# Performance work log

Hardware: AMD Instinct MI355X
Metric: run time of the kernel (lower is better)

## Reference

```python
import jax, jax.numpy as jnp
import numpy as np

N_NODES = 20000
IN_CH = 128
OUT_CH = 128
HEADS = 1
OB_DIM = 4
N_STEP = 32           # = HEADS*OUT_CH*8 // 32
D_PE = 16             # 32 - HEADS*16
N_EDGES = 256000


def setup_inputs() -> dict:
    key = jax.random.key(0)
    ks = jax.random.split(key, 9)
    x = jax.random.normal(ks[0], (N_NODES, IN_CH), jnp.float32)
    p_t = jax.random.normal(ks[1], (N_STEP, D_PE), jnp.float32)
    edge_index = jax.random.randint(ks[2], (2, N_EDGES), 0, N_NODES, jnp.int32)
    edge_weights = jax.random.uniform(ks[3], (N_EDGES,), jnp.float32)
    # Linear params (PyTorch default init: U(-1/sqrt(fan_in), 1/sqrt(fan_in)))
    s = 1.0 / np.sqrt(IN_CH)
    lin_value_w = jax.random.uniform(ks[4], (IN_CH, HEADS * OUT_CH), jnp.float32, -s, s)
    lin_value_b = jax.random.uniform(ks[5], (HEADS * OUT_CH,), jnp.float32, -s, s)
    inc_w = jax.random.uniform(ks[6], (IN_CH, HEADS * OUT_CH * 8), jnp.float32, -s, s)
    inc_b = jax.random.uniform(ks[7], (HEADS * OUT_CH * 8,), jnp.float32, -s, s)
    g = np.sqrt(6.0 / (N_NODES + HEADS * 16))  # glorot
    map_weights = jax.random.uniform(ks[8], (N_NODES, HEADS * 16), jnp.float32, -g, g)
    return {"x": x, "p_t": p_t, "edge_index": edge_index, "edge_weights": edge_weights,
            "lin_value_w": lin_value_w, "lin_value_b": lin_value_b,
            "inc_w": inc_w, "inc_b": inc_b, "map_weights": map_weights}


def _segment_softmax(gamma, index, num_segments):
    # PyG-style softmax over edges grouped by destination index, per column
    m = jax.ops.segment_max(gamma, index, num_segments=num_segments)     # [N, D]
    num = jnp.exp(gamma - m[index])
    den = jax.ops.segment_sum(num, index, num_segments=num_segments)    # [N, D]
    return num / den[index]


def reference(x, p_t, edge_index, edge_weights, lin_value_w, lin_value_b,
              inc_w, inc_b, map_weights):
    src = edge_index[0]   # x_j side
    dst = edge_index[1]   # x_i side (flow source_to_target)
    n_step = p_t.shape[0]
    E = src.shape[0]

    x_i = x[dst]                                             # [E, in]
    # h_W = increase_dim(x_i).view(E, n_step, 32)
    h_W = (x_i @ inc_w + inc_b).reshape(E, n_step, 32)       # [E, T, 32]
    w_v = map_weights[dst]                                   # [E, 16]
    # beta = mean(h_W * cat([w_v, p_t], -1), -1) computed without materializing aa
    beta = (jnp.einsum('etk,ek->et', h_W[:, :, :16], w_v)
            + jnp.einsum('etk,tk->et', h_W[:, :, 16:], p_t)) / 32.0   # [E, T]

    gamma = beta * edge_weights[:, None]                     # [E, T]
    gamma = jnp.repeat(gamma, OB_DIM, axis=-1)               # [E, T*ob_dim] = [E, H*out]
    all_edge_weights = jnp.mean(gamma, axis=1)               # [E]

    K = int(E * 0.5)
    _, top_idx = jax.lax.top_k(all_edge_weights, K)          # top-K edges
    gamma = gamma[top_idx]                                   # [K, H*out]
    x_i = x_i[top_idx]                                       # [K, in]
    # NOTE: the module re-points aggregation index to edge_index[0] (source)
    index = src[top_idx]                                     # [K]

    gamma = _segment_softmax(gamma, index, N_NODES)          # [K, H*out]

    v = jax.nn.relu(x_i @ lin_value_w + lin_value_b)         # [K, H*out]
    msg = (v.reshape(K, HEADS, OUT_CH)
           * gamma.reshape(K, HEADS, OUT_CH))                # [K, H, out]

    out = jax.ops.segment_sum(msg.reshape(K, HEADS * OUT_CH), index,
                              num_segments=N_NODES)          # scatter-add
    return out                                               # [N, H*out]
```

## Files before the change

kernel.cpp:

```cpp
#include <hip/hip_runtime.h>

#define NN 20000
#define IC 128
#define OC 128
#define NSTEP 32
#define NE 256000
#define KSEL 128000
#define NB 79
#define CANDCAP 131072
#define NQCOL 704

struct SelState {
  unsigned long long prefix;
  unsigned r;
  unsigned selc;
  unsigned tiec;
  unsigned done[8];
};

typedef __attribute__((ext_vector_type(16))) float f16v;

__global__ void k_init(const float* __restrict__ p_t, const float* __restrict__ lin_w,
                       const float* __restrict__ lin_b,
                       const float* __restrict__ inc_w, const float* __restrict__ inc_b,
                       float* __restrict__ Wq,
                       double* __restrict__ Ud, double* __restrict__ ubd,
                       unsigned* __restrict__ cnt, unsigned* __restrict__ hist,
                       SelState* st) {
  int i = blockIdx.x * blockDim.x + threadIdx.x;
  if (i < 33 * NQCOL) {
    int k4 = i / NQCOL, col = i - k4 * NQCOL;
    float4 o;
    float* ov = (float*)&o;
    for (int jj = 0; jj < 4; ++jj) {
      int k = 4 * k4 + jj;
      float v = 0.f;
      if (col < 512) {
        int t = col >> 4, c = col & 15;
        if (k < 128) v = inc_w[k * 1024 + t * 32 + c];
        else if (k == 128) v = inc_b[t * 32 + c];
      } else if (col < 544) {
        int t = col - 512;
        if (k < 128) {
          float a = 0.f;
          for (int q = 0; q < 16; ++q) a += inc_w[k * 1024 + t * 32 + 16 + q] * p_t[t * 16 + q];
          v = a;
        } else if (k == 128) {
          float a = 0.f;
          for (int q = 0; q < 16; ++q) a += inc_b[t * 32 + 16 + q] * p_t[t * 16 + q];
          v = a;
        }
      } else if (col < 672) {
        int c = col - 544;
        if (k < 128) v = lin_w[k * OC + c];
        else if (k == 128) v = lin_b[c];
      }
      ov[jj] = v;
    }
    ((float4*)Wq)[i] = o;
    return;
  }
  i -= 33 * NQCOL;
  if (i < 17 * IC) {
    int c = i >> 7, k = i & 127;
    double a = 0.0;
    if (c < 16) {
      for (int t = 0; t < NSTEP; ++t) a += (double)inc_w[k * 1024 + t * 32 + c];
    } else {
      for (int t = 0; t < NSTEP; ++t)
        for (int q = 0; q < 16; ++q)
          a += (double)inc_w[k * 1024 + t * 32 + 16 + q] * (double)p_t[t * 16 + q];
    }
    Ud[c * IC + k] = a;
    return;
  }
  i -= 17 * IC;
  if (i < 17) {
    double a = 0.0;
    if (i < 16) {
      for (int t = 0; t < NSTEP; ++t) a += (double)inc_b[t * 32 + i];
    } else {
      for (int t = 0; t < NSTEP; ++t)
        for (int q = 0; q < 16; ++q)
          a += (double)inc_b[t * 32 + 16 + q] * (double)p_t[t * 16 + q];
    }
    ubd[i] = a;
    return;
  }
  i -= 17;
  if (i < NN) { cnt[i] = 0u; return; }
  i -= NN;
  if (i < 512) { hist[i] = 0u; return; }
  i -= 512;
  if (i == 0) {
    st->prefix = 0ull; st->r = KSEL; st->selc = 0u; st->tiec = 0u;
    for (int p = 0; p < 8; ++p) st->done[p] = 0u;
  }
}

#define FMA4(WV, BASE)                                                                        \
  acc[BASE+0] = fmaf(xf.x, WV[0],  fmaf(xf.y, WV[1],  fmaf(xf.z, WV[2],  fmaf(xf.w, WV[3],  acc[BASE+0])))); \
  acc[BASE+1] = fmaf(xf.x, WV[4],  fmaf(xf.y, WV[5],  fmaf(xf.z, WV[6],  fmaf(xf.w, WV[7],  acc[BASE+1])))); \
  acc[BASE+2] = fmaf(xf.x, WV[8],  fmaf(xf.y, WV[9],  fmaf(xf.z, WV[10], fmaf(xf.w, WV[11], acc[BASE+2])))); \
  acc[BASE+3] = fmaf(xf.x, WV[12], fmaf(xf.y, WV[13], fmaf(xf.z, WV[14], fmaf(xf.w, WV[15], acc[BASE+3]))));

__global__ __launch_bounds__(256) void k_node(
    const float* __restrict__ x, const float* __restrict__ mw,
    const float* __restrict__ Wq,
    float* __restrict__ beta, float* __restrict__ V) {
  __shared__ float4 xl[64 * 32];
  int tid = threadIdx.x;
  int g = blockIdx.x;
  int s = blockIdx.y;
  int n0 = g * 64;
  int nvalid = NN - n0; if (nvalid > 64) nvalid = 64;

  for (int i = tid; i < 64 * 32; i += 256) {
    int mm = i >> 5, k4 = i & 31;
    float4 v = make_float4(0.f, 0.f, 0.f, 0.f);
    if (mm < nvalid) v = ((const float4*)(x + (size_t)(n0 + mm) * IC))[k4];
    xl[(mm << 5) + ((k4 + mm) & 31)] = v;
  }
  int m = tid & 63;
  int j = __builtin_amdgcn_readfirstlane(threadIdx.x >> 6);
  __syncthreads();

  for (int r = 0; r < 2; ++r) {
    int u = s * 8 + j + r * 4;
    if (u < 32) {
      float mwr[16];
      {
        int mm = (m < nvalid) ? m : 0;
        const float4* mp = (const float4*)(mw + (size_t)(n0 + mm) * 16);
#pragma unroll
        for (int i = 0; i < 4; ++i) {
          float4 t4 = mp[i];
          mwr[4 * i] = t4.x; mwr[4 * i + 1] = t4.y; mwr[4 * i + 2] = t4.z; mwr[4 * i + 3] = t4.w;
        }
      }
      const f16v*   wb = (const f16v*)Wq + (u << 2);
      const float4* wp = (const float4*)Wq + (512 + u);
      float acc[16], accp;
      {
        const f16v* wkb = wb + 32 * 176;
        f16v b0 = wkb[0], b1 = wkb[1], b2 = wkb[2], b3 = wkb[3];
#pragma unroll
        for (int c = 0; c < 4; ++c) {
          acc[c] = b0[4 * c]; acc[4 + c] = b1[4 * c];
          acc[8 + c] = b2[4 * c]; acc[12 + c] = b3[4 * c];
        }
        accp = wp[32 * NQCOL].x;
      }
      f16v w0 = wb[0], w1 = wb[1], w2 = wb[2], w3 = wb[3];
      float4 pw = wp[0];
      for (int k4 = 0; k4 < 32; ++k4) {
        f16v nw0, nw1, nw2, nw3; float4 npw;
        if (k4 < 31) {
          const f16v* wn = wb + (k4 + 1) * 176;
          nw0 = wn[0]; nw1 = wn[1]; nw2 = wn[2]; nw3 = wn[3];
          npw = wp[(k4 + 1) * NQCOL];
        }
        float4 xf = xl[(m << 5) + ((k4 + m) & 31)];
        FMA4(w0, 0) FMA4(w1, 4) FMA4(w2, 8) FMA4(w3, 12)
        accp = fmaf(xf.x, pw.x, fmaf(xf.y, pw.y, fmaf(xf.z, pw.z, fmaf(xf.w, pw.w, accp))));
        if (k4 < 31) { w0 = nw0; w1 = nw1; w2 = nw2; w3 = nw3; pw = npw; }
      }
      float bs = accp;
#pragma unroll
      for (int c = 0; c < 16; ++c) bs = fmaf(acc[c], mwr[c], bs);
      if (m < nvalid) beta[(size_t)(n0 + m) * NSTEP + u] = bs * (1.f / 32.f);
    } else {
      int vg = u - 32;
      int vc0 = vg << 4;
      const f16v* wb = (const f16v*)Wq + 136 + (vg << 2);
      float acc[16];
      {
        const f16v* wkb = wb + 32 * 176;
        f16v b0 = wkb[0], b1 = wkb[1], b2 = wkb[2], b3 = wkb[3];
#pragma unroll
        for (int c = 0; c < 4; ++c) {
          acc[c] = b0[4 * c]; acc[4 + c] = b1[4 * c];
          acc[8 + c] = b2[4 * c]; acc[12 + c] = b3[4 * c];
        }
      }
      f16v w0 = wb[0], w1 = wb[1], w2 = wb[2], w3 = wb[3];
      for (int k4 = 0; k4 < 32; ++k4) {
        f16v nw0, nw1, nw2, nw3;
        if (k4 < 31) {
          const f16v* wn = wb + (k4 + 1) * 176;
          nw0 = wn[0]; nw1 = wn[1]; nw2 = wn[2]; nw3 = wn[3];
        }
        float4 xf = xl[(m << 5) + ((k4 + m) & 31)];
        FMA4(w0, 0) FMA4(w1, 4) FMA4(w2, 8) FMA4(w3, 12)
        if (k4 < 31) { w0 = nw0; w1 = nw1; w2 = nw2; w3 = nw3; }
      }
      if (m < nvalid) {
        float* vout = V + (size_t)(n0 + m) * OC + vc0;
#pragma unroll
        for (int q = 0; q < 4; ++q) {
          float4 o;
          o.x = fmaxf(acc[4 * q], 0.f);     o.y = fmaxf(acc[4 * q + 1], 0.f);
          o.z = fmaxf(acc[4 * q + 2], 0.f); o.w = fmaxf(acc[4 * q + 3], 0.f);
          ((float4*)vout)[q] = o;
        }
      }
    }
  }
}

__global__ __launch_bounds__(256) void k_s64(
    const float* __restrict__ x, const float* __restrict__ mw,
    const double* __restrict__ Ud, const double* __restrict__ ubd,
    double* __restrict__ s64) {
  __shared__ float4 xl[64 * 32];
  __shared__ double sdd[64][18];
  int tid = threadIdx.x;
  int n0 = blockIdx.x * 64;
  int nvalid = NN - n0; if (nvalid > 64) nvalid = 64;

  for (int i = tid; i < 64 * 32; i += 256) {
    int mm = i >> 5, k4 = i & 31;
    float4 v = make_float4(0.f, 0.f, 0.f, 0.f);
    if (mm < nvalid) v = ((const float4*)(x + (size_t)(n0 + mm) * IC))[k4];
    xl[(mm << 5) + ((k4 + mm) & 31)] = v;
  }
  __syncthreads();
  int m = tid & 63, j = tid >> 6;
  for (int c = j; c < 17; c += 4) {
    const double* uc = Ud + c * IC;
    double a0 = 0.0, a1 = 0.0, a2 = 0.0, a3 = 0.0;
    for (int k4 = 0; k4 < 32; ++k4) {
      float4 xv = xl[(m << 5) + ((k4 + m) & 31)];
      a0 = fma((double)xv.x, uc[4 * k4],     a0);
      a1 = fma((double)xv.y, uc[4 * k4 + 1], a1);
      a2 = fma((double)xv.z, uc[4 * k4 + 2], a2);
      a3 = fma((double)xv.w, uc[4 * k4 + 3], a3);
    }
    sdd[m][c] = (a0 + a1) + (a2 + a3);
  }
  __syncthreads();
  if (tid < 64 && tid < nvalid) {
    const float* mp = mw + (size_t)(n0 + tid) * 16;
    double ssum = sdd[tid][16] + ubd[16];
#pragma unroll
    for (int c = 0; c < 16; ++c) ssum += (sdd[tid][c] + ubd[c]) * (double)mp[c];
    s64[n0 + tid] = ssum * (1.0 / 1024.0);
  }
}

__global__ void k_key(const int* __restrict__ ei, const float* __restrict__ ew,
                      const double* __restrict__ s64,
                      unsigned long long* __restrict__ keys,
                      unsigned* __restrict__ hist, SelState* st) {
  __shared__ unsigned h[256], suf[256];
  __shared__ int last;
  int tid = threadIdx.x;
  h[tid] = 0u;
  if (tid == 0) last = 0;
  __syncthreads();
  for (int e = blockIdx.x * 256 + tid; e < NE; e += gridDim.x * 256) {
    int d = ei[NE + e];
    double v = s64[d] * (double)ew[e];
    unsigned long long u = (unsigned long long)__double_as_longlong(v);
    u = (u & 0x8000000000000000ull) ? ~u : (u | 0x8000000000000000ull);
    keys[e] = u;
    atomicAdd(&h[(unsigned)(u >> 56)], 1u);
  }
  __syncthreads();
  if (h[tid]) atomicAdd(&hist[tid], h[tid]);
  __threadfence();
  __syncthreads();
  if (tid == 0) {
    unsigned old = atomicAdd(&st->done[0], 1u);
    if (old == gridDim.x - 1) last = 1;
  }
  __syncthreads();
  if (!last) return;
  unsigned c = atomicAdd(&hist[tid], 0u);
  suf[tid] = c;
  __syncthreads();
  for (int d = 1; d < 256; d <<= 1) {
    unsigned v = (tid + d < 256) ? suf[tid + d] : 0u;
    __syncthreads();
    suf[tid] += v;
    __syncthreads();
  }
  unsigned r = st->r;
  unsigned exc = suf[tid] - c;
  if (exc < r && exc + c >= r) {
    st->prefix = (unsigned long long)tid;
    st->r = r - exc;
  }
}

__global__ void k_radix(const unsigned long long* __restrict__ keys,
                        unsigned* __restrict__ hist, SelState* st, int p) {
  __shared__ unsigned h[256], suf[256];
  __shared__ int last;
  int tid = threadIdx.x;
  h[tid] = 0u;
  if (tid == 0) last = 0;
  unsigned long long pref = st->prefix;
  __syncthreads();
  int shift = 56 - 8 * p;
  unsigned* hp = hist + p * 256;
  for (int e = blockIdx.x * 256 + tid; e < NE; e += gridDim.x * 256) {
    unsigned long long k = keys[e];
    if ((k >> (shift + 8)) == pref)
      atomicAdd(&h[(unsigned)((k >> shift) & 255ull)], 1u);
  }
  __syncthreads();
  if (h[tid]) atomicAdd(&hp[tid], h[tid]);
  __threadfence();
  __syncthreads();
  if (tid == 0) {
    unsigned old = atomicAdd(&st->done[p], 1u);
    if (old == gridDim.x - 1) last = 1;
  }
  __syncthreads();
  if (!last) return;
  unsigned c = atomicAdd(&hp[tid], 0u);
  suf[tid] = c;
  __syncthreads();
  for (int d = 1; d < 256; d <<= 1) {
    unsigned v = (tid + d < 256) ? suf[tid + d] : 0u;
    __syncthreads();
    suf[tid] += v;
    __syncthreads();
  }
  unsigned r = st->r;
  unsigned exc = suf[tid] - c;
  if (exc < r && exc + c >= r) {
    st->prefix = (st->prefix << 8) | (unsigned long long)tid;
    st->r = r - exc;
  }
}

__global__ void k_cand(const unsigned long long* __restrict__ keys, SelState* st,
                       unsigned long long* __restrict__ candk, int* __restrict__ cande) {
  int e = blockIdx.x * 256 + threadIdx.x;
  if (e >= NE) return;
  unsigned long long k = keys[e];
  if ((unsigned)(k >> 48) == (unsigned)st->prefix) {
    unsigned pos = atomicAdd(&st->tiec, 1u);
    if (pos < CANDCAP) { candk[pos] = k; cande[pos] = e; }
  }
}

__global__ void k_sel(const unsigned long long* __restrict__ candk,
                      const int* __restrict__ cande, const int* __restrict__ ei,
                      SelState* st, int* __restrict__ sel, unsigned* __restrict__ cnt) {
  __shared__ unsigned h[256], suf[256];
  __shared__ unsigned long long spref;
  __shared__ unsigned sr;
  int tid = threadIdx.x;
  unsigned C = st->tiec; if (C > CANDCAP) C = CANDCAP;
  if (tid == 0) { spref = st->prefix; sr = st->r; }
  __syncthreads();
  for (int p = 2; p < 8; ++p) {
    h[tid] = 0u;
    __syncthreads();
    int shift = 56 - 8 * p;
    unsigned long long pf = spref;
    unsigned r = sr;
    for (unsigned i = tid; i < C; i += 256) {
      unsigned long long k = candk[i];
      if ((k >> (shift + 8)) == pf) atomicAdd(&h[(unsigned)((k >> shift) & 255ull)], 1u);
    }
    __syncthreads();
    suf[tid] = h[tid];
    __syncthreads();
    for (int d = 1; d < 256; d <<= 1) {
      unsigned v = (tid + d < 256) ? suf[tid + d] : 0u;
      __syncthreads();
      suf[tid] += v;
      __syncthreads();
    }
    unsigned exc = suf[tid] - h[tid];
    if (exc < r && exc + h[tid] >= r) {
      spref = (pf << 8) | (unsigned long long)tid;
      sr = r - exc;
    }
    __syncthreads();
  }
  unsigned long long T = spref;
  unsigned needed = sr;
  if (tid == 0) { st->prefix = T; st->r = needed; }
  for (unsigned i = tid; i < C; i += 256) {
    if (candk[i] == T) {
      int e = cande[i];
      unsigned rank = 0;
      for (unsigned q = 0; q < C; ++q)
        rank += (candk[q] == T && cande[q] < e) ? 1u : 0u;
      if (rank < needed) {
        unsigned pos = atomicAdd(&st->selc, 1u);
        if (pos < KSEL) { sel[pos] = e; atomicAdd(&cnt[ei[e]], 1u); }
      }
    }
  }
}

__global__ void k_compact(const unsigned long long* __restrict__ keys,
                          const int* __restrict__ ei, SelState* st,
                          int* __restrict__ sel, unsigned* __restrict__ cnt) {
  int e = blockIdx.x * 256 + threadIdx.x;
  if (e >= NE) return;
  if (keys[e] > st->prefix) {
    unsigned pos = atomicAdd(&st->selc, 1u);
    if (pos < KSEL) { sel[pos] = e; atomicAdd(&cnt[ei[e]], 1u); }
  }
}

__global__ void k_pref1(const unsigned* __restrict__ cnt, unsigned* __restrict__ bsum) {
  __shared__ unsigned sd[256];
  int i = blockIdx.x * 256 + threadIdx.x;
  sd[threadIdx.x] = (i < NN) ? cnt[i] : 0u;
  __syncthreads();
  for (int s = 128; s > 0; s >>= 1) {
    if (threadIdx.x < s) sd[threadIdx.x] += sd[threadIdx.x + s];
    __syncthreads();
  }
  if (threadIdx.x == 0) bsum[blockIdx.x] = sd[0];
}

__global__ void k_pref2(const unsigned* __restrict__ bsum, unsigned* __restrict__ bbase,
                        unsigned* __restrict__ offar) {
  __shared__ unsigned sd[128];
  int tid = threadIdx.x;
  unsigned v = (tid < NB) ? bsum[tid] : 0u;
  sd[tid] = v;
  __syncthreads();
  for (int d = 1; d < 128; d <<= 1) {
    unsigned u = (tid >= d) ? sd[tid - d] : 0u;
    __syncthreads();
    sd[tid] += u;
    __syncthreads();
  }
  if (tid < NB) bbase[tid] = sd[tid] - v;
  if (tid == NB - 1) offar[NN] = sd[tid];
}

__global__ void k_pref3(const unsigned* __restrict__ cnt, const unsigned* __restrict__ bbase,
                        unsigned* __restrict__ offar, unsigned* __restrict__ cursor) {
  __shared__ unsigned sd[256];
  int tid = threadIdx.x;
  int i = blockIdx.x * 256 + tid;
  unsigned v = (i < NN) ? cnt[i] : 0u;
  sd[tid] = v;
  __syncthreads();
  for (int d = 1; d < 256; d <<= 1) {
    unsigned u = (tid >= d) ? sd[tid - d] : 0u;
    __syncthreads();
    sd[tid] += u;
    __syncthreads();
  }
  if (i < NN) {
    unsigned excl = bbase[blockIdx.x] + sd[tid] - v;
    offar[i] = excl;
    cursor[i] = excl;
  }
}

__global__ void k_scatter(const int* __restrict__ sel, const int* __restrict__ ei,
                          unsigned* __restrict__ cursor, int* __restrict__ csr) {
  int i = blockIdx.x * 256 + threadIdx.x;
  if (i >= KSEL) return;
  int e = sel[i];
  unsigned pos = atomicAdd(&cursor[ei[e]], 1u);
  if (pos < KSEL) csr[pos] = e;
}

__global__ __launch_bounds__(128) void k_out(
    const int* __restrict__ ei, const float* __restrict__ ew,
    const float* __restrict__ beta, const float* __restrict__ V,
    const unsigned* __restrict__ offar, const int* __restrict__ csr,
    float* __restrict__ out) {
  __shared__ float B[32][NSTEP];
  __shared__ float m[NSTEP], den[NSTEP], scale[NSTEP];
  __shared__ int dl[32];
  __shared__ float ewl[32];
  int n = blockIdx.x, tid = threadIdx.x;
  unsigned beg = offar[n], end = offar[n + 1];
  if (end > (unsigned)KSEL) end = KSEL;
  if (beg > end) beg = end;
  if (tid < NSTEP) { m[tid] = -INFINITY; den[tid] = 0.f; }
  float acc = 0.f;
  int c = tid, tq = tid >> 2;
  __syncthreads();

  for (unsigned cb = beg; cb < end; cb += 32u) {
    unsigned ce = end - cb; if (ce > 32u) ce = 32u;
    if (tid < (int)ce) {
      int e = csr[cb + tid];
      dl[tid] = ei[NE + e];
      ewl[tid] = ew[e];
    }
    __syncthreads();
    for (int idx = tid; idx < (int)ce * NSTEP; idx += 128) {
      int el = idx >> 5, t = idx & 31;
      B[el][t] = beta[(size_t)dl[el] * NSTEP + t] * ewl[el];
    }
    __syncthreads();
    if (tid < NSTEP) {
      int t = tid;
      float mc = -INFINITY;
      for (int el = 0; el < (int)ce; ++el) mc = fmaxf(mc, B[el][t]);
      float mnew = fmaxf(m[t], mc);
      float sc = expf(m[t] - mnew);
      float s = 0.f;
      for (int el = 0; el < (int)ce; ++el) {
        float g = expf(B[el][t] - mnew);
        B[el][t] = g;
        s += g;
      }
      den[t] = den[t] * sc + s;
      m[t] = mnew;
      scale[t] = sc;
    }
    __syncthreads();
    acc *= scale[tq];
    for (int el = 0; el < (int)ce; ++el)
      acc += V[(size_t)dl[el] * OC + c] * B[el][tq];
    __syncthreads();
  }
  float d = den[tq];
  out[(size_t)n * OC + c] = (d > 0.f) ? acc / d : 0.f;
}

extern "C" void kernel_launch(void* const* d_in, const int* in_sizes, int n_in,
                              void* d_out, int out_size, void* d_ws, size_t ws_size,
                              hipStream_t stream) {
  const float* x     = (const float*)d_in[0];
  const float* p_t   = (const float*)d_in[1];
  const int*   ei    = (const int*)d_in[2];
  const float* ew    = (const float*)d_in[3];
  const float* lin_w = (const float*)d_in[4];
  const float* lin_b = (const float*)d_in[5];
  const float* inc_w = (const float*)d_in[6];
  const float* inc_b = (const float*)d_in[7];
  const float* mw    = (const float*)d_in[8];
  float* out = (float*)d_out;

  char* w = (char*)d_ws;
  size_t off = 0;
  auto alloc = [&](size_t b) -> void* {
    void* p = w + off;
    off += (b + 511) & ~(size_t)511;
    return p;
  };
  float*  Wq    = (float*)alloc((size_t)33 * NQCOL * 4 * 4);
  double* Ud    = (double*)alloc((size_t)17 * IC * 8);
  double* ubd   = (double*)alloc(17 * 8);
  float*  beta  = (float*)alloc((size_t)NN * NSTEP * 4);
  double* s64   = (double*)alloc((size_t)NN * 8);
  float*  V     = (float*)alloc((size_t)NN * OC * 4);
  unsigned long long* keys  = (unsigned long long*)alloc((size_t)NE * 8);
  unsigned long long* candk = (unsigned long long*)alloc((size_t)CANDCAP * 8);
  int*      cande  = (int*)alloc((size_t)CANDCAP * 4);
  int*      sel    = (int*)alloc((size_t)KSEL * 4);
  unsigned* cnt    = (unsigned*)alloc((size_t)NN * 4);
  unsigned* offar  = (unsigned*)alloc((size_t)(NN + 1) * 4);
  unsigned* cursor = (unsigned*)alloc((size_t)NN * 4);
  int*      csr    = (int*)alloc((size_t)KSEL * 4);
  unsigned* hist   = (unsigned*)alloc(512 * 4);
  unsigned* bsum   = (unsigned*)alloc(NB * 4);
  unsigned* bbase  = (unsigned*)alloc(NB * 4);
  SelState* st     = (SelState*)alloc(sizeof(SelState));
  if (off > ws_size) return;

  int init_threads = 33 * NQCOL + 17 * IC + 17 + NN + 512 + 1;
  k_init<<<(init_threads + 255) / 256, 256, 0, stream>>>(p_t, lin_w, lin_b, inc_w, inc_b,
                                                         Wq, Ud, ubd, cnt, hist, st);
  k_node<<<dim3((NN + 63) / 64, 5), 256, 0, stream>>>(x, mw, Wq, beta, V);
  k_s64<<<(NN + 63) / 64, 256, 0, stream>>>(x, mw, Ud, ubd, s64);
  k_key<<<256, 256, 0, stream>>>(ei, ew, s64, keys, hist, st);
  k_radix<<<256, 256, 0, stream>>>(keys, hist, st, 1);
  k_cand<<<(NE + 255) / 256, 256, 0, stream>>>(keys, st, candk, cande);
  k_sel<<<1, 256, 0, stream>>>(candk, cande, ei, st, sel, cnt);
  k_compact<<<(NE + 255) / 256, 256, 0, stream>>>(keys, ei, st, sel, cnt);
  k_pref1<<<NB, 256, 0, stream>>>(cnt, bsum);
  k_pref2<<<1, 128, 0, stream>>>(bsum, bbase, offar);
  k_pref3<<<NB, 256, 0, stream>>>(cnt, bbase, offar, cursor);
  k_scatter<<<(KSEL + 255) / 256, 256, 0, stream>>>(sel, ei, cursor, csr);
  k_out<<<NN, 128, 0, stream>>>(ei, ew, beta, V, offar, csr, out);
}
```

Baseline: 339.4 us.

## Fuse top-K radix selection passes and prefix kernels with last-block completion

The top-K selection now builds one 16-bit global histogram in a single pass in place of two 8-bit passes. Candidate collection, strict-greater compaction and the tie-breaking refinement are merged into one kernel that uses a last-block-done pattern, and the first two prefix-sum kernels are merged the same way. k_s64 is rewritten to use 16 threads per node with a shuffle reduction instead of shared-memory tiling. The goal is fewer kernel launches and fewer full passes over the keys. The cost is contention from global atomics on a 64K-bin histogram and the extra work of zeroing that larger histogram.

```diff
diff --git a/kernel.cpp b/kernel.cpp
--- a/kernel.cpp
+++ b/kernel.cpp
@@ -9,6 +9,7 @@
 #define NB 79
 #define CANDCAP 131072
 #define NQCOL 704
+#define HISTN 65536
 
 struct SelState {
   unsigned long long prefix;
@@ -90,8 +91,8 @@
   i -= 17;
   if (i < NN) { cnt[i] = 0u; return; }
   i -= NN;
-  if (i < 512) { hist[i] = 0u; return; }
-  i -= 512;
+  if (i < HISTN) { hist[i] = 0u; return; }
+  i -= HISTN;
   if (i == 0) {
     st->prefix = 0ull; st->r = KSEL; st->selc = 0u; st->tiec = 0u;
     for (int p = 0; p < 8; ++p) st->done[p] = 0u;
@@ -212,72 +213,58 @@
     const float* __restrict__ x, const float* __restrict__ mw,
     const double* __restrict__ Ud, const double* __restrict__ ubd,
     double* __restrict__ s64) {
-  __shared__ float4 xl[64 * 32];
-  __shared__ double sdd[64][18];
+  int tid = blockIdx.x * 256 + threadIdx.x;
+  int m = tid >> 4, c = tid & 15;
+  if (m >= NN) return;
+  const float*  xr  = x + (size_t)m * IC;
+  const double* uc  = Ud + c * IC;
+  const double* u16 = Ud + 16 * IC;
+  double a = 0.0, a16 = 0.0;
+  for (int k = 0; k < IC; k += 4) {
+    float4 xv = *(const float4*)(xr + k);
+    a   = fma((double)xv.x, uc[k],      a);
+    a   = fma((double)xv.y, uc[k + 1],  a);
+    a   = fma((double)xv.z, uc[k + 2],  a);
+    a   = fma((double)xv.w, uc[k + 3],  a);
+    a16 = fma((double)xv.x, u16[k],     a16);
+    a16 = fma((double)xv.y, u16[k + 1], a16);
+    a16 = fma((double)xv.z, u16[k + 2], a16);
+    a16 = fma((double)xv.w, u16[k + 3], a16);
+  }
+  double part = (a + ubd[c]) * (double)mw[m * 16 + c];
+#pragma unroll
+  for (int d = 1; d < 16; d <<= 1) part += __shfl_xor(part, d, 64);
+  if (c == 0) s64[m] = (part + a16 + ubd[16]) * (1.0 / 1024.0);
+}
+
+__global__ void k_keysel(const int* __restrict__ ei, const float* __restrict__ ew,
+                         const double* __restrict__ s64,
+                         unsigned long long* __restrict__ keys,
+                         unsigned* __restrict__ hist, SelState* st) {
+  __shared__ unsigned suf[256];
+  __shared__ int last, cch;
+  __shared__ unsigned cexc;
   int tid = threadIdx.x;
-  int n0 = blockIdx.x * 64;
-  int nvalid = NN - n0; if (nvalid > 64) nvalid = 64;
-
-  for (int i = tid; i < 64 * 32; i += 256) {
-    int mm = i >> 5, k4 = i & 31;
-    float4 v = make_float4(0.f, 0.f, 0.f, 0.f);
-    if (mm < nvalid) v = ((const float4*)(x + (size_t)(n0 + mm) * IC))[k4];
-    xl[(mm << 5) + ((k4 + mm) & 31)] = v;
-  }
-  __syncthreads();
-  int m = tid & 63, j = tid >> 6;
-  for (int c = j; c < 17; c += 4) {
-    const double* uc = Ud + c * IC;
-    double a0 = 0.0, a1 = 0.0, a2 = 0.0, a3 = 0.0;
-    for (int k4 = 0; k4 < 32; ++k4) {
-      float4 xv = xl[(m << 5) + ((k4 + m) & 31)];
-      a0 = fma((double)xv.x, uc[4 * k4],     a0);
-      a1 = fma((double)xv.y, uc[4 * k4 + 1], a1);
-      a2 = fma((double)xv.z, uc[4 * k4 + 2], a2);
-      a3 = fma((double)xv.w, uc[4 * k4 + 3], a3);
-    }
-    sdd[m][c] = (a0 + a1) + (a2 + a3);
-  }
-  __syncthreads();
-  if (tid < 64 && tid < nvalid) {
-    const float* mp = mw + (size_t)(n0 + tid) * 16;
-    double ssum = sdd[tid][16] + ubd[16];
-#pragma unroll
-    for (int c = 0; c < 16; ++c) ssum += (sdd[tid][c] + ubd[c]) * (double)mp[c];
-    s64[n0 + tid] = ssum * (1.0 / 1024.0);
-  }
-}
-
-__global__ void k_key(const int* __restrict__ ei, const float* __restrict__ ew,
-                      const double* __restrict__ s64,
-                      unsigned long long* __restrict__ keys,
-                      unsigned* __restrict__ hist, SelState* st) {
-  __shared__ unsigned h[256], suf[256];
-  __shared__ int last;
-  int tid = threadIdx.x;
-  h[tid] = 0u;
   if (tid == 0) last = 0;
-  __syncthreads();
   for (int e = blockIdx.x * 256 + tid; e < NE; e += gridDim.x * 256) {
     int d = ei[NE + e];
     double v = s64[d] * (double)ew[e];
     unsigned long long u = (unsigned long long)__double_as_longlong(v);
     u = (u & 0x8000000000000000ull) ? ~u : (u | 0x8000000000000000ull);
     keys[e] = u;
-    atomicAdd(&h[(unsigned)(u >> 56)], 1u);
-  }
-  __syncthreads();
-  if (h[tid]) atomicAdd(&hist[tid], h[tid]);
+    atomicAdd(&hist[(unsigned)(u >> 48)], 1u);
+  }
   __threadfence();
   __syncthreads();
   if (tid == 0) {
-    unsigned old = atomicAdd(&st->done[0], 1u);
-    if (old == gridDim.x - 1) last = 1;
+    if (atomicAdd(&st->done[0], 1u) == gridDim.x - 1) last = 1;
   }
   __syncthreads();
   if (!last) return;
-  unsigned c = atomicAdd(&hist[tid], 0u);
-  suf[tid] = c;
+  unsigned csum = 0;
+  int base = tid << 8;
+  for (int b = 0; b < 256; ++b) csum += hist[base + b];
+  suf[tid] = csum;
   __syncthreads();
   for (int d = 1; d < 256; d <<= 1) {
     unsigned v = (tid + d < 256) ? suf[tid + d] : 0u;
@@ -285,42 +272,13 @@
     suf[tid] += v;
     __syncthreads();
   }
-  unsigned r = st->r;
-  unsigned exc = suf[tid] - c;
-  if (exc < r && exc + c >= r) {
-    st->prefix = (unsigned long long)tid;
-    st->r = r - exc;
-  }
-}
-
-__global__ void k_radix(const unsigned long long* __restrict__ keys,
-                        unsigned* __restrict__ hist, SelState* st, int p) {
-  __shared__ unsigned h[256], suf[256];
-  __shared__ int last;
-  int tid = threadIdx.x;
-  h[tid] = 0u;
-  if (tid == 0) last = 0;
-  unsigned long long pref = st->prefix;
-  __syncthreads();
-  int shift = 56 - 8 * p;
-  unsigned* hp = hist + p * 256;
-  for (int e = blockIdx.x * 256 + tid; e < NE; e += gridDim.x * 256) {
-    unsigned long long k = keys[e];
-    if ((k >> (shift + 8)) == pref)
-      atomicAdd(&h[(unsigned)((k >> shift) & 255ull)], 1u);
-  }
-  __syncthreads();
-  if (h[tid]) atomicAdd(&hp[tid], h[tid]);
-  __threadfence();
-  __syncthreads();
-  if (tid == 0) {
-    unsigned old = atomicAdd(&st->done[p], 1u);
-    if (old == gridDim.x - 1) last = 1;
-  }
-  __syncthreads();
-  if (!last) return;
-  unsigned c = atomicAdd(&hp[tid], 0u);
-  suf[tid] = c;
+  {
+    unsigned exc = suf[tid] - csum;
+    if (exc < KSEL && exc + csum >= KSEL) { cch = tid; cexc = exc; }
+  }
+  __syncthreads();
+  unsigned h2 = hist[(cch << 8) + tid];
+  suf[tid] = h2;
   __syncthreads();
   for (int d = 1; d < 256; d <<= 1) {
     unsigned v = (tid + d < 256) ? suf[tid + d] : 0u;
@@ -328,34 +286,46 @@
     suf[tid] += v;
     __syncthreads();
   }
-  unsigned r = st->r;
-  unsigned exc = suf[tid] - c;
-  if (exc < r && exc + c >= r) {
-    st->prefix = (st->prefix << 8) | (unsigned long long)tid;
-    st->r = r - exc;
-  }
-}
-
-__global__ void k_cand(const unsigned long long* __restrict__ keys, SelState* st,
-                       unsigned long long* __restrict__ candk, int* __restrict__ cande) {
-  int e = blockIdx.x * 256 + threadIdx.x;
-  if (e >= NE) return;
-  unsigned long long k = keys[e];
-  if ((unsigned)(k >> 48) == (unsigned)st->prefix) {
-    unsigned pos = atomicAdd(&st->tiec, 1u);
-    if (pos < CANDCAP) { candk[pos] = k; cande[pos] = e; }
-  }
-}
-
-__global__ void k_sel(const unsigned long long* __restrict__ candk,
-                      const int* __restrict__ cande, const int* __restrict__ ei,
-                      SelState* st, int* __restrict__ sel, unsigned* __restrict__ cnt) {
+  {
+    unsigned exc2 = cexc + (suf[tid] - h2);
+    if (exc2 < KSEL && exc2 + h2 >= KSEL) {
+      st->prefix = (unsigned long long)((cch << 8) + tid);
+      st->r = KSEL - exc2;
+    }
+  }
+}
+
+__global__ void k_candsel(const unsigned long long* __restrict__ keys,
+                          const int* __restrict__ ei, SelState* st,
+                          int* __restrict__ sel, unsigned* __restrict__ cnt,
+                          unsigned long long* __restrict__ candk, int* __restrict__ cande) {
   __shared__ unsigned h[256], suf[256];
   __shared__ unsigned long long spref;
   __shared__ unsigned sr;
+  __shared__ int last;
   int tid = threadIdx.x;
-  unsigned C = st->tiec; if (C > CANDCAP) C = CANDCAP;
-  if (tid == 0) { spref = st->prefix; sr = st->r; }
+  if (tid == 0) last = 0;
+  unsigned P16 = (unsigned)st->prefix;
+  for (int e = blockIdx.x * 256 + tid; e < NE; e += gridDim.x * 256) {
+    unsigned long long k = keys[e];
+    unsigned t16 = (unsigned)(k >> 48);
+    if (t16 > P16) {
+      unsigned pos = atomicAdd(&st->selc, 1u);
+      if (pos < KSEL) { sel[pos] = e; atomicAdd(&cnt[ei[e]], 1u); }
+    } else if (t16 == P16) {
+      unsigned pos = atomicAdd(&st->tiec, 1u);
+      if (pos < CANDCAP) { candk[pos] = k; cande[pos] = e; }
+    }
+  }
+  __threadfence();
+  __syncthreads();
+  if (tid == 0) {
+    if (atomicAdd(&st->done[1], 1u) == gridDim.x - 1) last = 1;
+  }
+  __syncthreads();
+  if (!last) return;
+  unsigned C = atomicAdd(&st->tiec, 0u); if (C > CANDCAP) C = CANDCAP;
+  if (tid == 0) { spref = (unsigned long long)P16; sr = st->r; }
   __syncthreads();
   for (int p = 2; p < 8; ++p) {
     h[tid] = 0u;
@@ -385,9 +355,13 @@
   }
   unsigned long long T = spref;
   unsigned needed = sr;
-  if (tid == 0) { st->prefix = T; st->r = needed; }
   for (unsigned i = tid; i < C; i += 256) {
-    if (candk[i] == T) {
+    unsigned long long k = candk[i];
+    if (k > T) {
+      int e = cande[i];
+      unsigned pos = atomicAdd(&st->selc, 1u);
+      if (pos < KSEL) { sel[pos] = e; atomicAdd(&cnt[ei[e]], 1u); }
+    } else if (k == T) {
       int e = cande[i];
       unsigned rank = 0;
       for (unsigned q = 0; q < C; ++q)
@@ -400,37 +374,32 @@
   }
 }
 
-__global__ void k_compact(const unsigned long long* __restrict__ keys,
-                          const int* __restrict__ ei, SelState* st,
-                          int* __restrict__ sel, unsigned* __restrict__ cnt) {
-  int e = blockIdx.x * 256 + threadIdx.x;
-  if (e >= NE) return;
-  if (keys[e] > st->prefix) {
-    unsigned pos = atomicAdd(&st->selc, 1u);
-    if (pos < KSEL) { sel[pos] = e; atomicAdd(&cnt[ei[e]], 1u); }
-  }
-}
-
-__global__ void k_pref1(const unsigned* __restrict__ cnt, unsigned* __restrict__ bsum) {
+__global__ void k_pref12(const unsigned* __restrict__ cnt, unsigned* __restrict__ bsum,
+                         unsigned* __restrict__ bbase, unsigned* __restrict__ offar,
+                         SelState* st) {
   __shared__ unsigned sd[256];
-  int i = blockIdx.x * 256 + threadIdx.x;
-  sd[threadIdx.x] = (i < NN) ? cnt[i] : 0u;
+  __shared__ int last;
+  int tid = threadIdx.x;
+  if (tid == 0) last = 0;
+  int i = blockIdx.x * 256 + tid;
+  sd[tid] = (i < NN) ? cnt[i] : 0u;
   __syncthreads();
   for (int s = 128; s > 0; s >>= 1) {
-    if (threadIdx.x < s) sd[threadIdx.x] += sd[threadIdx.x + s];
-    __syncthreads();
-  }
-  if (threadIdx.x == 0) bsum[blockIdx.x] = sd[0];
-}
-
-__global__ void k_pref2(const unsigned* __restrict__ bsum, unsigned* __restrict__ bbase,
-                        unsigned* __restrict__ offar) {
-  __shared__ unsigned sd[128];
-  int tid = threadIdx.x;
+    if (tid < s) sd[tid] += sd[tid + s];
+    __syncthreads();
+  }
+  if (tid == 0) bsum[blockIdx.x] = sd[0];
+  __threadfence();
+  __syncthreads();
+  if (tid == 0) {
+    if (atomicAdd(&st->done[2], 1u) == gridDim.x - 1) last = 1;
+  }
+  __syncthreads();
+  if (!last) return;
   unsigned v = (tid < NB) ? bsum[tid] : 0u;
   sd[tid] = v;
   __syncthreads();
-  for (int d = 1; d < 128; d <<= 1) {
+  for (int d = 1; d < 256; d <<= 1) {
     unsigned u = (tid >= d) ? sd[tid - d] : 0u;
     __syncthreads();
     sd[tid] += u;
@@ -562,24 +531,20 @@
   unsigned* offar  = (unsigned*)alloc((size_t)(NN + 1) * 4);
   unsigned* cursor = (unsigned*)alloc((size_t)NN * 4);
   int*      csr    = (int*)alloc((size_t)KSEL * 4);
-  unsigned* hist   = (unsigned*)alloc(512 * 4);
+  unsigned* hist   = (unsigned*)alloc((size_t)HISTN * 4);
   unsigned* bsum   = (unsigned*)alloc(NB * 4);
   unsigned* bbase  = (unsigned*)alloc(NB * 4);
   SelState* st     = (SelState*)alloc(sizeof(SelState));
   if (off > ws_size) return;
 
-  int init_threads = 33 * NQCOL + 17 * IC + 17 + NN + 512 + 1;
+  int init_threads = 33 * NQCOL + 17 * IC + 17 + NN + HISTN + 1;
   k_init<<<(init_threads + 255) / 256, 256, 0, stream>>>(p_t, lin_w, lin_b, inc_w, inc_b,
                                                          Wq, Ud, ubd, cnt, hist, st);
   k_node<<<dim3((NN + 63) / 64, 5), 256, 0, stream>>>(x, mw, Wq, beta, V);
-  k_s64<<<(NN + 63) / 64, 256, 0, stream>>>(x, mw, Ud, ubd, s64);
-  k_key<<<256, 256, 0, stream>>>(ei, ew, s64, keys, hist, st);
-  k_radix<<<256, 256, 0, stream>>>(keys, hist, st, 1);
-  k_cand<<<(NE + 255) / 256, 256, 0, stream>>>(keys, st, candk, cande);
-  k_sel<<<1, 256, 0, stream>>>(candk, cande, ei, st, sel, cnt);
-  k_compact<<<(NE + 255) / 256, 256, 0, stream>>>(keys, ei, st, sel, cnt);
-  k_pref1<<<NB, 256, 0, stream>>>(cnt, bsum);
-  k_pref2<<<1, 128, 0, stream>>>(bsum, bbase, offar);
+  k_s64<<<(NN * 16 + 255) / 256, 256, 0, stream>>>(x, mw, Ud, ubd, s64);
+  k_keysel<<<256, 256, 0, stream>>>(ei, ew, s64, keys, hist, st);
+  k_candsel<<<256, 256, 0, stream>>>(keys, ei, st, sel, cnt, candk, cande);
+  k_pref12<<<NB, 256, 0, stream>>>(cnt, bsum, bbase, offar, st);
   k_pref3<<<NB, 256, 0, stream>>>(cnt, bbase, offar, cursor);
   k_scatter<<<(KSEL + 255) / 256, 256, 0, stream>>>(sel, ei, cursor, csr);
   k_out<<<NN, 128, 0, stream>>>(ei, ew, beta, V, offar, csr, out);
```

Result: slower. 479.8 us (+41.4%).
